# Kernel optimization log

Hardware: AMD Instinct MI355X
Metric: run time of the kernel (lower is better)

Reference implementation:

```python
import jax, jax.numpy as jnp
import numpy as np

MASK_FILL = -987654321.0


def rotate_every_two(x):
    # pairs (x0, x1) -> (-x1, x0), interleaved back along last dim
    x1 = x[..., 0::2]
    x2 = x[..., 1::2]
    return jnp.stack((-x2, x1), axis=-1).reshape(x.shape)


def setup_inputs() -> dict:
    key = jax.random.key(0)
    ks = jax.random.split(key, 6)
    b, n, dim = 64, 197, 768
    heads, dim_head = 12, 64
    inner = heads * dim_head
    x = jax.random.normal(ks[0], (b, n, dim), dtype=jnp.float32)
    pos_emb = jax.random.normal(ks[1], (1, n, dim_head), dtype=jnp.float32)
    w_qkv = jax.random.normal(ks[2], (dim, 3 * inner), dtype=jnp.float32) * (dim ** -0.5)
    scale = jnp.full((heads,), dim_head ** -0.5, dtype=jnp.float32)
    w_out = jax.random.normal(ks[3], (inner, dim), dtype=jnp.float32) * (inner ** -0.5)
    b_out = jnp.zeros((dim,), dtype=jnp.float32)
    return {"x": x, "pos_emb": pos_emb, "w_qkv": w_qkv, "scale": scale,
            "w_out": w_out, "b_out": b_out}


def reference(x, pos_emb, w_qkv, scale, w_out, b_out):
    b, n, dim = x.shape
    h = scale.shape[0]
    qkv = x @ w_qkv                         # [b, n, 3*inner]
    q, k, v = jnp.split(qkv, 3, axis=-1)
    dh = q.shape[-1] // h
    to_heads = lambda t: t.reshape(b, n, h, dh).transpose(0, 2, 1, 3)  # bhnd
    q, k, v = to_heads(q), to_heads(k), to_heads(v)

    # RoPE: pos_emb [1, n, (2 * dh/2)] -> sin/cos [n, dh/2] -> interleave to [n, dh]
    sc = pos_emb[0].reshape(n, 2, dh // 2)
    sin = jnp.repeat(sc[:, 0], 2, axis=-1)  # [n, dh]
    cos = jnp.repeat(sc[:, 1], 2, axis=-1)
    q = q * cos + rotate_every_two(q) * sin
    k = k * cos + rotate_every_two(k) * sin

    # per-head learnable scale
    dots = jnp.einsum('bhid,bhjd->bhij', q, k) * scale[None, :, None, None]
    # diagonal (LSA) mask
    eye = jnp.eye(n, dtype=bool)
    dots = jnp.where(eye, MASK_FILL, dots)

    attn = jax.nn.softmax(dots, axis=-1)
    out = jnp.einsum('bhij,bhjd->bhid', attn, v)
    out = out.transpose(0, 2, 1, 3).reshape(b, n, h * dh)
    return out @ w_out + b_out
```

## Files before the change

### kernel.cpp

```cpp
#include <hip/hip_runtime.h>
#include <math.h>

#define MASK_FILL_F (-987654321.0f)

typedef unsigned short u16;
typedef unsigned int   u32;

constexpr int Bb   = 64;
constexpr int Ntok = 197;
constexpr int Dim  = 768;
constexpr int Heads= 12;
constexpr int Dh   = 64;
constexpr int Nq3  = 2304;
constexpr int Rows = 12608;
constexpr int Mpad = 12672;

using f32x4  = __attribute__((ext_vector_type(4))) float;
using bf16x8 = __attribute__((ext_vector_type(8))) short;

__device__ __forceinline__ u16 f2bf(float f) {
  u32 u = __float_as_uint(f);
  u = (u + 0x7fffu + ((u >> 16) & 1u)) >> 16;
  return (u16)u;
}

__device__ __forceinline__ void stage16(const void* gp, void* lp) {
  __builtin_amdgcn_global_load_lds(
      (const __attribute__((address_space(1))) u32*)gp,
      (__attribute__((address_space(3))) u32*)lp, 16, 0, 0);
}

__global__ __launch_bounds__(256) void cvt_bf16(const float* __restrict__ in,
                                                u16* __restrict__ out, int n4) {
  const int i = blockIdx.x * 256 + threadIdx.x;
  if (i < n4) {
    const float4 v = *(const float4*)&in[(size_t)i * 4];
    ushort4 u;
    u.x = f2bf(v.x); u.y = f2bf(v.y); u.z = f2bf(v.z); u.w = f2bf(v.w);
    *(ushort4*)&out[(size_t)i * 4] = u;
  }
}

__global__ __launch_bounds__(256) void transpose_cvt(const float* __restrict__ in,
                                                     u16* __restrict__ out,
                                                     int R, int C) {
  __shared__ float t[32][33];
  const int c0 = blockIdx.x * 32, r0 = blockIdx.y * 32;
  const int tx = threadIdx.x & 31, ty = threadIdx.x >> 5;
#pragma unroll
  for (int rr = ty; rr < 32; rr += 8)
    t[rr][tx] = in[(size_t)(r0 + rr) * C + c0 + tx];
  __syncthreads();
#pragma unroll
  for (int cc = ty; cc < 32; cc += 8)
    out[(size_t)(c0 + cc) * R + r0 + tx] = f2bf(t[tx][cc]);
}

template<int MODE>
__global__ __launch_bounds__(256) void gemm_bt(
    const u16* __restrict__ Ag, const u16* __restrict__ Bg,
    void* __restrict__ Cv, int K, int Nn,
    const float* __restrict__ pe, const float* __restrict__ bias)
{
  __shared__ u16 As[128 * 32];
  __shared__ u16 Bs[128 * 32];
  const int tid = threadIdx.x, lane = tid & 63, w = tid >> 6;
  const int m0 = blockIdx.y * 128, n0 = blockIdx.x * 128;
  const int wm = (w & 1) * 64, wn = (w >> 1) * 64;
  const int tx = lane & 15, qk = lane >> 4;
  const int rs = lane >> 2, cs = (lane & 3) * 8;

  f32x4 acc[4][4] = {};

  for (int k0 = 0; k0 < K; k0 += 32) {
#pragma unroll
    for (int t = 0; t < 2; ++t) {
      const int r0 = w * 16 + t * 64;
      stage16(Ag + (size_t)(m0 + r0 + rs) * K + k0 + cs, &As[r0 * 32]);
      stage16(Bg + (size_t)(n0 + r0 + rs) * K + k0 + cs, &Bs[r0 * 32]);
    }
    __syncthreads();
    bf16x8 af[4], bf[4];
#pragma unroll
    for (int f = 0; f < 4; ++f) {
      af[f] = *(const bf16x8*)&As[(wm + f * 16 + tx) * 32 + qk * 8];
      bf[f] = *(const bf16x8*)&Bs[(wn + f * 16 + tx) * 32 + qk * 8];
    }
#pragma unroll
    for (int fm = 0; fm < 4; ++fm)
#pragma unroll
      for (int fn = 0; fn < 4; ++fn)
        acc[fm][fn] = __builtin_amdgcn_mfma_f32_16x16x32_bf16(
            af[fm], bf[fn], acc[fm][fn], 0, 0, 0);
    __syncthreads();
  }

  if (MODE == 0) {
    u16* C = (u16*)Cv;
    const bool dorot = (n0 < 2 * Dim);
#pragma unroll
    for (int fm = 0; fm < 4; ++fm) {
      const int rbase = m0 + wm + fm * 16 + qk * 4;
      int iq[4];
#pragma unroll
      for (int r = 0; r < 4; ++r) iq[r] = (rbase + r) % Ntok;
#pragma unroll
      for (int fn = 0; fn < 4; ++fn) {
        const int col = n0 + wn + fn * 16 + tx;
        const int mm  = (col & 63) >> 1;
        const int odd = col & 1;
#pragma unroll
        for (int r = 0; r < 4; ++r) {
          float v = acc[fm][fn][r];
          float res = v;
          if (dorot) {
            const float other = __shfl_xor(v, 1, 64);
            const float sn = pe[iq[r] * 64 + mm];
            const float c2 = pe[iq[r] * 64 + 32 + mm];
            res = odd ? (v * c2 + other * sn) : (v * c2 - other * sn);
          }
          C[(size_t)(rbase + r) * Nn + col] = f2bf(res);
        }
      }
    }
  } else {
    float* C = (float*)Cv;
#pragma unroll
    for (int fm = 0; fm < 4; ++fm) {
      const int rbase = m0 + wm + fm * 16 + qk * 4;
#pragma unroll
      for (int fn = 0; fn < 4; ++fn) {
        const int col = n0 + wn + fn * 16 + tx;
        const float bv = bias[col];
#pragma unroll
        for (int r = 0; r < 4; ++r) {
          const int row = rbase + r;
          if (row < Rows) C[(size_t)row * Nn + col] = acc[fm][fn][r] + bv;
        }
      }
    }
  }
}

constexpr int LS = 72;

__global__ __launch_bounds__(256) void attn4(
    const u16* __restrict__ qkvB, const float* __restrict__ scale,
    u16* __restrict__ outB)
{
  __shared__ u16 qs [64 * LS];
  __shared__ u16 ks [64 * LS];
  __shared__ u16 vts[64 * LS];

  const int it = blockIdx.x, bh = blockIdx.y;
  const int b = bh / Heads, h = bh % Heads;
  const int i0 = it * 64;
  const float sc = scale[h];
  const int tid = threadIdx.x, lane = tid & 63, w = tid >> 6;
  const int tx = lane & 15, q = lane >> 4;
  const size_t rowbase = (size_t)b * Ntok;

  for (int idx = tid; idx < 512; idx += 256) {
    const int r = idx >> 3, c8 = (idx & 7) * 8;
    *(uint4*)&qs[r * LS + c8] =
        *(const uint4*)(qkvB + (rowbase + i0 + r) * (size_t)Nq3 + h * Dh + c8);
  }

  float m_i = -3.0e38f, l_i = 0.f;
  f32x4 oacc[4] = {};

  for (int jt = 0; jt < 4; ++jt) {
    const int j0 = jt * 64;
    __syncthreads();

    for (int idx = tid; idx < 512; idx += 256) {
      const int r = idx >> 3, c8 = (idx & 7) * 8;
      *(uint4*)&ks[r * LS + c8] =
          *(const uint4*)(qkvB + (rowbase + j0 + r) * (size_t)Nq3 + Dim + h * Dh + c8);
    }
    for (int idx = tid; idx < 512; idx += 256) {
      const int c = idx & 63, dc = (idx >> 6) * 8;
      const int jj = 32 * (c >> 5) + 16 * ((c >> 2) & 1) + 4 * ((c >> 3) & 3) + (c & 3);
      const bool valid = (j0 + jj) < Ntok;
      const uint4 u = *(const uint4*)(qkvB + (rowbase + j0 + jj) * (size_t)Nq3 +
                                      2 * Dim + h * Dh + dc);
      const u16* e = (const u16*)&u;
#pragma unroll
      for (int t2 = 0; t2 < 8; ++t2)
        vts[(dc + t2) * LS + c] = valid ? e[t2] : (u16)0;
    }
    __syncthreads();

    f32x4 sT[4] = {};
#pragma unroll
    for (int kk = 0; kk < 2; ++kk) {
      const bf16x8 bq = *(const bf16x8*)&qs[(w * 16 + tx) * LS + kk * 32 + q * 8];
#pragma unroll
      for (int jb = 0; jb < 4; ++jb) {
        const bf16x8 ka = *(const bf16x8*)&ks[(jb * 16 + tx) * LS + kk * 32 + q * 8];
        sT[jb] = __builtin_amdgcn_mfma_f32_16x16x32_bf16(ka, bq, sT[jb], 0, 0, 0);
      }
    }

    const int ig = i0 + 16 * w + tx;
    float mrow = -3.0e38f;
#pragma unroll
    for (int jb = 0; jb < 4; ++jb)
#pragma unroll
      for (int r = 0; r < 4; ++r) {
        const int jg = j0 + 16 * jb + 4 * q + r;
        float s = sT[jb][r] * sc;
        if (jg >= Ntok) s = -3.0e38f;
        else if (jg == ig) s = MASK_FILL_F;
        sT[jb][r] = s;
        mrow = fmaxf(mrow, s);
      }
    mrow = fmaxf(mrow, __shfl_xor(mrow, 16, 64));
    mrow = fmaxf(mrow, __shfl_xor(mrow, 32, 64));
    const float mnew  = fmaxf(m_i, mrow);
    const float alpha = __expf(m_i - mnew);
    m_i = mnew;

    union { bf16x8 v; u16 e[8]; } pk[2];
    float lsum = 0.f;
#pragma unroll
    for (int jb = 0; jb < 4; ++jb)
#pragma unroll
      for (int r = 0; r < 4; ++r) {
        const float p = __expf(sT[jb][r] - mnew);
        lsum += p;
        pk[jb >> 1].e[(jb & 1) * 4 + r] = f2bf(p);
      }
    lsum += __shfl_xor(lsum, 16, 64);
    lsum += __shfl_xor(lsum, 32, 64);
    l_i = l_i * alpha + lsum;

#pragma unroll
    for (int r = 0; r < 4; ++r) {
      const float ar = __shfl(alpha, 4 * q + r, 64);
#pragma unroll
      for (int nb = 0; nb < 4; ++nb) oacc[nb][r] *= ar;
    }

#pragma unroll
    for (int kk = 0; kk < 2; ++kk)
#pragma unroll
      for (int nb = 0; nb < 4; ++nb) {
        const bf16x8 vb = *(const bf16x8*)&vts[(nb * 16 + tx) * LS + kk * 32 + q * 8];
        oacc[nb] = __builtin_amdgcn_mfma_f32_16x16x32_bf16(pk[kk].v, vb, oacc[nb], 0, 0, 0);
      }
  }

  const float linv = 1.0f / l_i;
#pragma unroll
  for (int r = 0; r < 4; ++r) {
    const float lr = __shfl(linv, 4 * q + r, 64);
    const int igr = i0 + 16 * w + 4 * q + r;
    if (igr < Ntok) {
#pragma unroll
      for (int nb = 0; nb < 4; ++nb)
        outB[(rowbase + igr) * (size_t)Dim + h * Dh + nb * 16 + tx] =
            f2bf(oacc[nb][r] * lr);
    }
  }
}

extern "C" void kernel_launch(void* const* d_in, const int* in_sizes, int n_in,
                              void* d_out, int out_size, void* d_ws, size_t ws_size,
                              hipStream_t stream) {
  const float* x     = (const float*)d_in[0];
  const float* pe    = (const float*)d_in[1];
  const float* w_qkv = (const float*)d_in[2];
  const float* scale = (const float*)d_in[3];
  const float* w_out = (const float*)d_in[4];
  const float* b_out = (const float*)d_in[5];
  float* out = (float*)d_out;

  u16* xb    = (u16*)d_ws;
  u16* wqkvT = xb    + (size_t)Mpad * Dim;
  u16* woutT = wqkvT + (size_t)Nq3 * Dim;
  u16* qkvB  = woutT + (size_t)Dim * Dim;
  u16* attnB = qkvB  + (size_t)Mpad * Nq3;

  cvt_bf16<<<(Rows * Dim / 4 + 255) / 256, 256, 0, stream>>>(x, xb, Rows * Dim / 4);
  transpose_cvt<<<dim3(Nq3 / 32, Dim / 32), 256, 0, stream>>>(w_qkv, wqkvT, Dim, Nq3);
  transpose_cvt<<<dim3(Dim / 32, Dim / 32), 256, 0, stream>>>(w_out, woutT, Dim, Dim);

  gemm_bt<0><<<dim3(Nq3 / 128, Mpad / 128), 256, 0, stream>>>(
      xb, wqkvT, qkvB, Dim, Nq3, pe, nullptr);

  attn4<<<dim3(4, Bb * Heads), 256, 0, stream>>>(qkvB, scale, attnB);

  gemm_bt<1><<<dim3(Dim / 128, Mpad / 128), 256, 0, stream>>>(
      attnB, woutT, out, Dim, Dim, nullptr, b_out);
}
```

Baseline: 284.9 us.

## Pre-transpose V in separate kernel and double query rows per attention block

```diff
diff --git a/kernel.cpp b/kernel.cpp
--- a/kernel.cpp
+++ b/kernel.cpp
@@ -30,6 +30,11 @@
       (__attribute__((address_space(3))) u32*)lp, 16, 0, 0);
 }
 
+__device__ __forceinline__ int sigma6(int M) {
+  return (M & 0x23) | (((M >> 3) & 1) << 4) | (((M >> 2) & 1) << 3) |
+         (((M >> 4) & 1) << 2);
+}
+
 __global__ __launch_bounds__(256) void cvt_bf16(const float* __restrict__ in,
                                                 u16* __restrict__ out, int n4) {
   const int i = blockIdx.x * 256 + threadIdx.x;
@@ -54,6 +59,36 @@
 #pragma unroll
   for (int cc = ty; cc < 32; cc += 8)
     out[(size_t)(c0 + cc) * R + r0 + tx] = f2bf(t[tx][cc]);
+}
+
+__global__ __launch_bounds__(256) void vtrans(const u16* __restrict__ qkvB,
+                                              u16* __restrict__ vT) {
+  __shared__ u16 t[64 * 72];
+  const int jt = blockIdx.x, bh = blockIdx.y;
+  const int b = bh / Heads, h = bh % Heads;
+  const int j0 = jt * 64;
+  const int tid = threadIdx.x;
+
+  for (int idx = tid; idx < 512; idx += 256) {
+    const int jr = idx >> 3, c8 = (idx & 7) * 8;
+    const int j = j0 + jr;
+    uint4 u = make_uint4(0u, 0u, 0u, 0u);
+    if (j < Ntok)
+      u = *(const uint4*)(qkvB + (size_t)(b * Ntok + j) * Nq3 + 2 * Dim + h * Dh + c8);
+    *(uint4*)&t[jr * 72 + c8] = u;
+  }
+  __syncthreads();
+  for (int idx = tid; idx < 512; idx += 256) {
+    const int d = idx >> 3, j8 = (idx & 7) * 8;
+    ushort4 lo, hi;
+    lo.x = t[(j8 + 0) * 72 + d]; lo.y = t[(j8 + 1) * 72 + d];
+    lo.z = t[(j8 + 2) * 72 + d]; lo.w = t[(j8 + 3) * 72 + d];
+    hi.x = t[(j8 + 4) * 72 + d]; hi.y = t[(j8 + 5) * 72 + d];
+    hi.z = t[(j8 + 6) * 72 + d]; hi.w = t[(j8 + 7) * 72 + d];
+    u16* dst = vT + ((size_t)bh * 64 + d) * 256 + j0 + j8;
+    *(ushort4*)dst       = lo;
+    *(ushort4*)(dst + 4) = hi;
+  }
 }
 
 template<int MODE>
@@ -144,123 +179,124 @@
 
 constexpr int LS = 72;
 
-__global__ __launch_bounds__(256) void attn4(
-    const u16* __restrict__ qkvB, const float* __restrict__ scale,
-    u16* __restrict__ outB)
+__global__ __launch_bounds__(256) void attn5(
+    const u16* __restrict__ qkvB, const u16* __restrict__ vT,
+    const float* __restrict__ scale, u16* __restrict__ outB)
 {
-  __shared__ u16 qs [64 * LS];
   __shared__ u16 ks [64 * LS];
   __shared__ u16 vts[64 * LS];
 
   const int it = blockIdx.x, bh = blockIdx.y;
   const int b = bh / Heads, h = bh % Heads;
-  const int i0 = it * 64;
+  const int i0 = it * 128;
   const float sc = scale[h];
   const int tid = threadIdx.x, lane = tid & 63, w = tid >> 6;
   const int tx = lane & 15, q = lane >> 4;
   const size_t rowbase = (size_t)b * Ntok;
 
-  for (int idx = tid; idx < 512; idx += 256) {
-    const int r = idx >> 3, c8 = (idx & 7) * 8;
-    *(uint4*)&qs[r * LS + c8] =
-        *(const uint4*)(qkvB + (rowbase + i0 + r) * (size_t)Nq3 + h * Dh + c8);
-  }
-
-  float m_i = -3.0e38f, l_i = 0.f;
-  f32x4 oacc[4] = {};
+  bf16x8 bq[2][2];
+#pragma unroll
+  for (int g = 0; g < 2; ++g)
+#pragma unroll
+    for (int kk = 0; kk < 2; ++kk)
+      bq[g][kk] = *(const bf16x8*)(qkvB +
+          (rowbase + i0 + 32 * w + 16 * g + tx) * (size_t)Nq3 + h * Dh + kk * 32 + q * 8);
+
+  float m_i[2] = {-3.0e38f, -3.0e38f}, l_i[2] = {0.f, 0.f};
+  f32x4 oacc[2][4] = {};
 
   for (int jt = 0; jt < 4; ++jt) {
     const int j0 = jt * 64;
     __syncthreads();
 
     for (int idx = tid; idx < 512; idx += 256) {
-      const int r = idx >> 3, c8 = (idx & 7) * 8;
-      *(uint4*)&ks[r * LS + c8] =
-          *(const uint4*)(qkvB + (rowbase + j0 + r) * (size_t)Nq3 + Dim + h * Dh + c8);
+      const int M = idx >> 3, c8 = (idx & 7) * 8;
+      const int js = sigma6(M);
+      *(uint4*)&ks[M * LS + c8] =
+          *(const uint4*)(qkvB + (rowbase + j0 + js) * (size_t)Nq3 + Dim + h * Dh + c8);
     }
     for (int idx = tid; idx < 512; idx += 256) {
-      const int c = idx & 63, dc = (idx >> 6) * 8;
-      const int jj = 32 * (c >> 5) + 16 * ((c >> 2) & 1) + 4 * ((c >> 3) & 3) + (c & 3);
-      const bool valid = (j0 + jj) < Ntok;
-      const uint4 u = *(const uint4*)(qkvB + (rowbase + j0 + jj) * (size_t)Nq3 +
-                                      2 * Dim + h * Dh + dc);
-      const u16* e = (const u16*)&u;
-#pragma unroll
-      for (int t2 = 0; t2 < 8; ++t2)
-        vts[(dc + t2) * LS + c] = valid ? e[t2] : (u16)0;
+      const int d = idx >> 3, c8 = (idx & 7) * 8;
+      *(uint4*)&vts[d * LS + c8] =
+          *(const uint4*)(vT + ((size_t)bh * 64 + d) * 256 + j0 + c8);
     }
     __syncthreads();
 
-    f32x4 sT[4] = {};
-#pragma unroll
-    for (int kk = 0; kk < 2; ++kk) {
-      const bf16x8 bq = *(const bf16x8*)&qs[(w * 16 + tx) * LS + kk * 32 + q * 8];
-#pragma unroll
-      for (int jb = 0; jb < 4; ++jb) {
-        const bf16x8 ka = *(const bf16x8*)&ks[(jb * 16 + tx) * LS + kk * 32 + q * 8];
-        sT[jb] = __builtin_amdgcn_mfma_f32_16x16x32_bf16(ka, bq, sT[jb], 0, 0, 0);
+#pragma unroll
+    for (int g = 0; g < 2; ++g) {
+      f32x4 sT[4] = {};
+#pragma unroll
+      for (int kk = 0; kk < 2; ++kk)
+#pragma unroll
+        for (int jb = 0; jb < 4; ++jb) {
+          const bf16x8 ka = *(const bf16x8*)&ks[(jb * 16 + tx) * LS + kk * 32 + q * 8];
+          sT[jb] = __builtin_amdgcn_mfma_f32_16x16x32_bf16(ka, bq[g][kk], sT[jb], 0, 0, 0);
+        }
+
+      const int ig = i0 + 32 * w + 16 * g + tx;
+      float mrow = -3.0e38f;
+#pragma unroll
+      for (int jb = 0; jb < 4; ++jb)
+#pragma unroll
+        for (int r = 0; r < 4; ++r) {
+          const int jg = j0 + 32 * (jb >> 1) + 8 * q + 4 * (jb & 1) + r;
+          float s = sT[jb][r] * sc;
+          if (jg >= Ntok) s = -3.0e38f;
+          else if (jg == ig) s = MASK_FILL_F;
+          sT[jb][r] = s;
+          mrow = fmaxf(mrow, s);
+        }
+      mrow = fmaxf(mrow, __shfl_xor(mrow, 16, 64));
+      mrow = fmaxf(mrow, __shfl_xor(mrow, 32, 64));
+      const float mnew  = fmaxf(m_i[g], mrow);
+      const float alpha = __expf(m_i[g] - mnew);
+      m_i[g] = mnew;
+
+      union { bf16x8 v; u16 e[8]; } pk[2];
+      float lsum = 0.f;
+#pragma unroll
+      for (int jb = 0; jb < 4; ++jb)
+#pragma unroll
+        for (int r = 0; r < 4; ++r) {
+          const float p = __expf(sT[jb][r] - mnew);
+          lsum += p;
+          pk[jb >> 1].e[(jb & 1) * 4 + r] = f2bf(p);
+        }
+      lsum += __shfl_xor(lsum, 16, 64);
+      lsum += __shfl_xor(lsum, 32, 64);
+      l_i[g] = l_i[g] * alpha + lsum;
+
+#pragma unroll
+      for (int r = 0; r < 4; ++r) {
+        const float ar = __shfl(alpha, 4 * q + r, 64);
+#pragma unroll
+        for (int nb = 0; nb < 4; ++nb) oacc[g][nb][r] *= ar;
       }
-    }
-
-    const int ig = i0 + 16 * w + tx;
-    float mrow = -3.0e38f;
-#pragma unroll
-    for (int jb = 0; jb < 4; ++jb)
-#pragma unroll
-      for (int r = 0; r < 4; ++r) {
-        const int jg = j0 + 16 * jb + 4 * q + r;
-        float s = sT[jb][r] * sc;
-        if (jg >= Ntok) s = -3.0e38f;
-        else if (jg == ig) s = MASK_FILL_F;
-        sT[jb][r] = s;
-        mrow = fmaxf(mrow, s);
+
+#pragma unroll
+      for (int kk = 0; kk < 2; ++kk)
+#pragma unroll
+        for (int nb = 0; nb < 4; ++nb) {
+          const bf16x8 vb = *(const bf16x8*)&vts[(nb * 16 + tx) * LS + kk * 32 + q * 8];
+          oacc[g][nb] = __builtin_amdgcn_mfma_f32_16x16x32_bf16(pk[kk].v, vb,
+                                                               oacc[g][nb], 0, 0, 0);
+        }
+    }
+  }
+
+#pragma unroll
+  for (int g = 0; g < 2; ++g) {
+    const float linv = 1.0f / l_i[g];
+#pragma unroll
+    for (int r = 0; r < 4; ++r) {
+      const float lr = __shfl(linv, 4 * q + r, 64);
+      const int igr = i0 + 32 * w + 16 * g + 4 * q + r;
+      if (igr < Ntok) {
+#pragma unroll
+        for (int nb = 0; nb < 4; ++nb)
+          outB[(rowbase + igr) * (size_t)Dim + h * Dh + nb * 16 + tx] =
+              f2bf(oacc[g][nb][r] * lr);
       }
-    mrow = fmaxf(mrow, __shfl_xor(mrow, 16, 64));
-    mrow = fmaxf(mrow, __shfl_xor(mrow, 32, 64));
-    const float mnew  = fmaxf(m_i, mrow);
-    const float alpha = __expf(m_i - mnew);
-    m_i = mnew;
-
-    union { bf16x8 v; u16 e[8]; } pk[2];
-    float lsum = 0.f;
-#pragma unroll
-    for (int jb = 0; jb < 4; ++jb)
-#pragma unroll
-      for (int r = 0; r < 4; ++r) {
-        const float p = __expf(sT[jb][r] - mnew);
-        lsum += p;
-        pk[jb >> 1].e[(jb & 1) * 4 + r] = f2bf(p);
-      }
-    lsum += __shfl_xor(lsum, 16, 64);
-    lsum += __shfl_xor(lsum, 32, 64);
-    l_i = l_i * alpha + lsum;
-
-#pragma unroll
-    for (int r = 0; r < 4; ++r) {
-      const float ar = __shfl(alpha, 4 * q + r, 64);
-#pragma unroll
-      for (int nb = 0; nb < 4; ++nb) oacc[nb][r] *= ar;
-    }
-
-#pragma unroll
-    for (int kk = 0; kk < 2; ++kk)
-#pragma unroll
-      for (int nb = 0; nb < 4; ++nb) {
-        const bf16x8 vb = *(const bf16x8*)&vts[(nb * 16 + tx) * LS + kk * 32 + q * 8];
-        oacc[nb] = __builtin_amdgcn_mfma_f32_16x16x32_bf16(pk[kk].v, vb, oacc[nb], 0, 0, 0);
-      }
-  }
-
-  const float linv = 1.0f / l_i;
-#pragma unroll
-  for (int r = 0; r < 4; ++r) {
-    const float lr = __shfl(linv, 4 * q + r, 64);
-    const int igr = i0 + 16 * w + 4 * q + r;
-    if (igr < Ntok) {
-#pragma unroll
-      for (int nb = 0; nb < 4; ++nb)
-        outB[(rowbase + igr) * (size_t)Dim + h * Dh + nb * 16 + tx] =
-            f2bf(oacc[nb][r] * lr);
     }
   }
 }
@@ -281,6 +317,7 @@
   u16* woutT = wqkvT + (size_t)Nq3 * Dim;
   u16* qkvB  = woutT + (size_t)Dim * Dim;
   u16* attnB = qkvB  + (size_t)Mpad * Nq3;
+  u16* vT    = attnB + (size_t)Mpad * Dim;
 
   cvt_bf16<<<(Rows * Dim / 4 + 255) / 256, 256, 0, stream>>>(x, xb, Rows * Dim / 4);
   transpose_cvt<<<dim3(Nq3 / 32, Dim / 32), 256, 0, stream>>>(w_qkv, wqkvT, Dim, Nq3);
@@ -289,7 +326,9 @@
   gemm_bt<0><<<dim3(Nq3 / 128, Mpad / 128), 256, 0, stream>>>(
       xb, wqkvT, qkvB, Dim, Nq3, pe, nullptr);
 
-  attn4<<<dim3(4, Bb * Heads), 256, 0, stream>>>(qkvB, scale, attnB);
+  vtrans<<<dim3(4, Bb * Heads), 256, 0, stream>>>(qkvB, vT);
+
+  attn5<<<dim3(2, Bb * Heads), 256, 0, stream>>>(qkvB, vT, scale, attnB);
 
   gemm_bt<1><<<dim3(Dim / 128, Mpad / 128), 256, 0, stream>>>(
       attnB, woutT, out, Dim, Dim, nullptr, b_out);
```

Measured after the change: 295.4 us. 3.7% more time.
